# Kernel tuning notes

Measured on AMD Instinct MI355X. Metric: run time of the kernel, lower is better.

The kernel has to match this reference:

```python
import jax, jax.numpy as jnp
import numpy as np
from jax import lax

D_TEMPORAL, D_INNER, D_STATE, D_CONV, DT_RANK = 2, 4, 16, 4, 1
EPS = 1e-5


def setup_inputs() -> dict:
    key = jax.random.key(0)
    ks = jax.random.split(key, 14)
    B, L = 16, 32768
    f = lambda k, s, scale=1.0: jax.random.normal(k, s, jnp.float32) * scale
    dt_b = float(np.log(np.expm1(0.01)))  # softplus^-1(0.01), typical dt init
    A_log = jnp.log(jnp.tile(jnp.arange(1, D_STATE + 1, dtype=jnp.float32), (D_INNER, 1)))
    return {
        "hidden_states": f(ks[0], (B, D_TEMPORAL, L)),
        "norm_w": jnp.ones((D_TEMPORAL,), jnp.float32),
        "in_proj_w": f(ks[1], (2 * D_INNER, D_TEMPORAL), 0.5),
        "conv_w": f(ks[2], (D_INNER, D_CONV), 0.3),
        "conv_b": f(ks[3], (D_INNER,), 0.1),
        "x_proj_w": f(ks[4], (DT_RANK + 2 * D_STATE, D_INNER), 0.3),
        "dt_proj_w": f(ks[5], (D_INNER, DT_RANK), 1.0),
        "dt_proj_b": jnp.full((D_INNER,), dt_b, jnp.float32),
        "A_log": A_log,
        "D": jnp.ones((D_INNER,), jnp.float32),
        "conv_w_b": f(ks[6], (D_INNER, D_CONV), 0.3),
        "conv_b_b": f(ks[7], (D_INNER,), 0.1),
        "x_proj_w_b": f(ks[8], (DT_RANK + 2 * D_STATE, D_INNER), 0.3),
        "dt_proj_w_b": f(ks[9], (D_INNER, DT_RANK), 1.0),
        "dt_proj_b_b": jnp.full((D_INNER,), dt_b, jnp.float32),
        "A_b_log": A_log,
        "D_b": jnp.ones((D_INNER,), jnp.float32),
        "out_proj_w": f(ks[10], (D_TEMPORAL, D_INNER), 0.3),
        "norm_f_w": jnp.ones((D_TEMPORAL,), jnp.float32),
    }


def _silu(x):
    return x * jax.nn.sigmoid(x)


def _rmsnorm(x, w):
    return x * lax.rsqrt(jnp.mean(x * x, axis=-1, keepdims=True) + EPS) * w


def _branch(x, z, conv_w, conv_b, x_proj_w, dt_proj_w, dt_proj_b, A_log, D):
    # x, z: (B, d_inner, L). Causal depthwise conv + silu.
    Bb, d, L = x.shape
    xc = lax.conv_general_dilated(
        x, conv_w[:, None, :], (1,), [(D_CONV - 1, 0)],
        feature_group_count=d, dimension_numbers=("NCH", "OIH", "NCH"))
    u = _silu(xc + conv_b[None, :, None]).transpose(0, 2, 1)      # (B, L, d)
    x_dbl = u @ x_proj_w.T                                        # (B, L, rank+2n)
    dt, Bm, Cm = jnp.split(x_dbl, [DT_RANK, DT_RANK + D_STATE], axis=-1)
    dt = jax.nn.softplus(dt @ dt_proj_w.T + dt_proj_b)            # (B, L, d)
    A = -jnp.exp(A_log)                                           # (d, n)
    dA = jnp.exp(dt[..., None] * A)                               # (B, L, d, n)
    dBu = (dt * u)[..., None] * Bm[:, :, None, :]                 # (B, L, d, n)

    def step(h, inp):
        dA_t, dBu_t, C_t = inp
        h = dA_t * h + dBu_t                                      # (B, d, n)
        return h, jnp.einsum("bdn,bn->bd", h, C_t)

    h0 = jnp.zeros((Bb, d, D_STATE), dtype=u.dtype)
    _, ys = lax.scan(step, h0, (jnp.swapaxes(dA, 0, 1), jnp.swapaxes(dBu, 0, 1), jnp.swapaxes(Cm, 0, 1)))
    y = jnp.swapaxes(ys, 0, 1) + u * D                            # (B, L, d)
    return y * _silu(z.transpose(0, 2, 1))


def _forward(hidden_states, norm_w, in_proj_w, conv_w, conv_b, x_proj_w, dt_proj_w,
             dt_proj_b, A_log, D, conv_w_b, conv_b_b, x_proj_w_b, dt_proj_w_b,
             dt_proj_b_b, A_b_log, D_b, out_proj_w, norm_f_w):
    # hidden_states: (B, T=d_temporal, L); scan runs over L.
    hs = jnp.swapaxes(hidden_states, 1, 2)                        # (B, L, T)
    residual = hs.astype(jnp.float32)
    hs = _rmsnorm(residual, norm_w)
    xz = jnp.swapaxes(hs @ in_proj_w.T, 1, 2)                     # (B, 2*d_inner, L)
    x, z = jnp.split(xz, 2, axis=1)
    y_f = _branch(x, z, conv_w, conv_b, x_proj_w, dt_proj_w, dt_proj_b, A_log, D)
    y_b = _branch(x[..., ::-1], z[..., ::-1], conv_w_b, conv_b_b, x_proj_w_b,
                  dt_proj_w_b, dt_proj_b_b, A_b_log, D_b)
    y = y_f + y_b[:, ::-1, :]                                     # (B, L, d_inner)
    out = y @ out_proj_w.T                                        # (B, L, T)
    out = _rmsnorm(out + residual, norm_f_w)
    return jnp.swapaxes(out, 1, 2)                                # (B, T, L)


def reference(hidden_states, norm_w, in_proj_w, conv_w, conv_b, x_proj_w, dt_proj_w,
              dt_proj_b, A_log, D, conv_w_b, conv_b_b, x_proj_w_b, dt_proj_w_b,
              dt_proj_b_b, A_b_log, D_b, out_proj_w, norm_f_w):
    return _forward(hidden_states, norm_w, in_proj_w, conv_w, conv_b, x_proj_w,
                    dt_proj_w, dt_proj_b, A_log, D, conv_w_b, conv_b_b, x_proj_w_b,
                    dt_proj_w_b, dt_proj_b_b, A_b_log, D_b, out_proj_w, norm_f_w)
```

## Files before the change

### kernel.cpp

```cpp
#include <hip/hip_runtime.h>
#include <cstdint>

#define BB 16
#define LL 32768
#define NC 512
#define NSPAN 32
#define SPLEN 16

#define WD_SZ 256
#define XPW 0
#define CVW 132
#define CVB 148
#define DTW 152
#define DTB 156
#define AW  160
#define DW  224
#define G_INPROJ 512
#define G_NORMW 528
#define G_OUTP 530
#define G_NORMF 538
#define FLG 1000

#define PQ_OFF 4096
#define PQ_BYTES ((size_t)BB*2*NC*64*8)
#define SP_OFF (PQ_OFF + PQ_BYTES)
#define SP_BYTES ((size_t)BB*2*NSPAN*64*8)
#define WG_OFF (SP_OFF + SP_BYTES)
#define WG_BYTES ((size_t)BB*NC*2*64*64*2)
#define YB_OFF (WG_OFF + WG_BYTES)
#define YB_BYTES ((size_t)BB*NC*64*4*4)

#define LOG2E 1.4426950408889634f

__device__ __forceinline__ float bf2f(unsigned short u){ return __uint_as_float(((unsigned int)u)<<16); }
__device__ __forceinline__ float blo(unsigned int u){ return __uint_as_float(u<<16); }
__device__ __forceinline__ float bhi(unsigned int u){ return __uint_as_float(u & 0xffff0000u); }

__device__ __forceinline__ unsigned int cvtpk(float lo, float hi){
  unsigned int r;
  asm("v_cvt_pk_bf16_f32 %0, %1, %2" : "=v"(r) : "v"(lo), "v"(hi));
  return r;
}
__device__ __forceinline__ unsigned short cvt1(float x){
  return (unsigned short)cvtpk(x, x);
}

__device__ __forceinline__ float siluf(float x){ return x / (1.f + __expf(-x)); }
__device__ __forceinline__ float softplusf_(float x){ return fmaxf(x,0.f) + log1pf(__expf(-fabsf(x))); }

__device__ __forceinline__ float exp2fast(float x){
#if __has_builtin(__builtin_amdgcn_exp2f)
  return __builtin_amdgcn_exp2f(x);
#else
  float r; asm("v_exp_f32 %0, %1\ns_nop 0" : "=v"(r) : "v"(x)); return r;
#endif
}

__device__ __forceinline__ float rowsum16(float x){
  asm("s_nop 1\n\t"
      "v_add_f32_dpp %0, %0, %0 row_ror:1 row_mask:0xf bank_mask:0xf\n\t"
      "s_nop 1\n\t"
      "v_add_f32_dpp %0, %0, %0 row_ror:2 row_mask:0xf bank_mask:0xf\n\t"
      "s_nop 1\n\t"
      "v_add_f32_dpp %0, %0, %0 row_ror:4 row_mask:0xf bank_mask:0xf\n\t"
      "s_nop 1\n\t"
      "v_add_f32_dpp %0, %0, %0 row_ror:8 row_mask:0xf bank_mask:0xf"
      : "+v"(x));
  return x;
}

__device__ __forceinline__ float ldw(const void* p, int i, int isf){
  return isf ? ((const float*)p)[i] : bf2f(((const unsigned short*)p)[i]);
}
__device__ __forceinline__ float2 hid2(const void* hid, int isf, int b, int t){
  if (isf){
    const float* p = (const float*)hid;
    return make_float2(p[(size_t)b*2*LL + t], p[(size_t)b*2*LL + LL + t]);
  }
  const unsigned short* p = (const unsigned short*)hid;
  return make_float2(bf2f(p[(size_t)b*2*LL + t]), bf2f(p[(size_t)b*2*LL + LL + t]));
}
__device__ __forceinline__ float4 xrow(const void* __restrict__ hid, int isf,
                                       const float* __restrict__ W, int b, int t){
  float2 h = hid2(hid, isf, b, t);
  float ms = rsqrtf(0.5f*(h.x*h.x + h.y*h.y) + 1e-5f);
  float v0 = h.x*ms*W[G_NORMW], v1 = h.y*ms*W[G_NORMW+1];
  float4 x;
  x.x = W[G_INPROJ+0]*v0 + W[G_INPROJ+1]*v1;
  x.y = W[G_INPROJ+2]*v0 + W[G_INPROJ+3]*v1;
  x.z = W[G_INPROJ+4]*v0 + W[G_INPROJ+5]*v1;
  x.w = W[G_INPROJ+6]*v0 + W[G_INPROJ+7]*v1;
  return x;
}

__global__ void k_prep(const void* __restrict__ normw, const void* __restrict__ inpj,
    const void* __restrict__ cwf, const void* __restrict__ cbf,
    const void* __restrict__ xpf, const void* __restrict__ dwf,
    const void* __restrict__ dbf, const void* __restrict__ alf,
    const void* __restrict__ ddf,
    const void* __restrict__ cwb, const void* __restrict__ cbb,
    const void* __restrict__ xpb, const void* __restrict__ dwb,
    const void* __restrict__ dbb, const void* __restrict__ alb,
    const void* __restrict__ ddb,
    const void* __restrict__ outp, const void* __restrict__ nfw,
    float* __restrict__ W)
{
  const int isf = (((const unsigned int*)ddf)[0] == 0x3F800000u) ? 1 : 0;
  int t = threadIdx.x;
  for (int i=t;i<132;i+=256){ W[XPW+i]=ldw(xpf,i,isf); W[WD_SZ+XPW+i]=ldw(xpb,i,isf); }
  for (int i=t;i<16;i+=256){ W[CVW+i]=ldw(cwf,i,isf); W[WD_SZ+CVW+i]=ldw(cwb,i,isf); W[G_INPROJ+i]=ldw(inpj,i,isf); }
  for (int i=t;i<4;i+=256){
    W[CVB+i]=ldw(cbf,i,isf); W[WD_SZ+CVB+i]=ldw(cbb,i,isf);
    W[DTW+i]=ldw(dwf,i,isf); W[WD_SZ+DTW+i]=ldw(dwb,i,isf);
    W[DTB+i]=ldw(dbf,i,isf); W[WD_SZ+DTB+i]=ldw(dbb,i,isf);
    W[DW+i] =ldw(ddf,i,isf); W[WD_SZ+DW+i] =ldw(ddb,i,isf);
  }
  for (int i=t;i<64;i+=256){
    W[AW+i]       = -__expf(ldw(alf,i,isf)) * LOG2E;
    W[WD_SZ+AW+i] = -__expf(ldw(alb,i,isf)) * LOG2E;
  }
  for (int i=t;i<8;i+=256) W[G_OUTP+i]=ldw(outp,i,isf);
  for (int i=t;i<2;i+=256){ W[G_NORMW+i]=ldw(normw,i,isf); W[G_NORMF+i]=ldw(nfw,i,isf); }
  if (t==0) W[FLG] = (float)isf;
}

template<int DR>
__device__ __forceinline__ float2 scan_store(const float (* __restrict__ dtPd)[68],
    const unsigned short (* __restrict__ dtud)[68],
    const unsigned int (* __restrict__ bcd)[68],
    float (* __restrict__ ySd)[68],
    unsigned short* __restrict__ wrow,
    float Ax, int d, int n, int dn)
{
  unsigned short* wr   = wrow + dn;
  unsigned short* wrHi = wr + 32*64;
  float P = 1.f, h = 0.f;
  for (int j4=0; j4<16; j4++){
    const int t0 = DR ? 60-4*j4 : 4*j4;
    float4  d4 = *(const float4*)&dtPd[d][t0];
    ushort4 u4 = *(const ushort4*)&dtud[d][t0];
    uint4   c4 = *(const uint4*)&bcd[n][t0];
    float da[4]={d4.x,d4.y,d4.z,d4.w};
    unsigned short ua[4]={u4.x,u4.y,u4.z,u4.w};
    unsigned int ca[4]={c4.x,c4.y,c4.z,c4.w};
    float s[4];
    #pragma unroll
    for (int jr=0; jr<4; jr++){
      const int k  = DR ? 3-jr : jr;
      const int tt = t0 + k;
      float e = exp2fast(Ax*da[k]);
      P *= e;
      float Cf = bhi(ca[k]);
      h = fmaf(e, h, bf2f(ua[k])*blo(ca[k]));
      ((tt < 32) ? wr : wrHi)[(tt & 31)*64] = cvt1(P*Cf);
      s[k] = rowsum16(h*Cf);
    }
    if (n == 0) *(float4*)&ySd[d][t0] = make_float4(s[0],s[1],s[2],s[3]);
  }
  return make_float2(P, h);
}

__global__ __launch_bounds__(128, 4) void k_chunk2(const void* __restrict__ hid,
    const float* __restrict__ W, float2* __restrict__ PQ,
    unsigned short* __restrict__ Wg, float4* __restrict__ YB)
{
  __shared__ __align__(16) char smx[2176];
  __shared__ __align__(16) float dtP[2][4][68];
  __shared__ __align__(16) unsigned short dtuP[2][4][68];
  __shared__ __align__(16) unsigned int BCp[2][16][68];
  __shared__ __align__(16) float uD[2][256];
  float4* xb = (float4*)smx;
  float (*yS)[4][68] = (float (*)[4][68])smx;

  const int tid  = threadIdx.x;
  const int wid  = tid >> 6;
  const int lane = tid & 63;
  const int gid  = blockIdx.x;
  const int c    = gid & (NC-1);
  const int b    = gid >> 9;
  const int isf  = (int)W[FLG];

  if (wid == 0){
    int t = c*64 + lane;
    xb[lane+3] = xrow(hid, isf, W, b, t);
    if (lane < 3){
      int t2 = c*64 - 3 + lane;
      float4 v = make_float4(0.f,0.f,0.f,0.f);
      if (t2 >= 0) v = xrow(hid, isf, W, b, t2);
      xb[lane] = v;
    }
    if (lane >= 61){
      int t3 = c*64 + lane + 3;
      float4 v = make_float4(0.f,0.f,0.f,0.f);
      if (t3 < LL) v = xrow(hid, isf, W, b, t3);
      xb[lane+6] = v;
    }
  }
  __syncthreads();
  {
    const float* Wd = W + wid*WD_SZ;
    float4 a0,a1,a2,a3;
    if (wid == 0){ a0=xb[lane];   a1=xb[lane+1]; a2=xb[lane+2]; a3=xb[lane+3]; }
    else         { a0=xb[lane+6]; a1=xb[lane+5]; a2=xb[lane+4]; a3=xb[lane+3]; }
    float u[4];
    u[0] = siluf(Wd[CVB+0] + Wd[CVW+ 0]*a0.x + Wd[CVW+ 1]*a1.x + Wd[CVW+ 2]*a2.x + Wd[CVW+ 3]*a3.x);
    u[1] = siluf(Wd[CVB+1] + Wd[CVW+ 4]*a0.y + Wd[CVW+ 5]*a1.y + Wd[CVW+ 6]*a2.y + Wd[CVW+ 7]*a3.y);
    u[2] = siluf(Wd[CVB+2] + Wd[CVW+ 8]*a0.z + Wd[CVW+ 9]*a1.z + Wd[CVW+10]*a2.z + Wd[CVW+11]*a3.z);
    u[3] = siluf(Wd[CVB+3] + Wd[CVW+12]*a0.w + Wd[CVW+13]*a1.w + Wd[CVW+14]*a2.w + Wd[CVW+15]*a3.w);
    float dtr = Wd[XPW+0]*u[0] + Wd[XPW+1]*u[1] + Wd[XPW+2]*u[2] + Wd[XPW+3]*u[3];
    float4 ud4;
    #pragma unroll
    for (int d2=0; d2<4; d2++){
      float dt = softplusf_(fmaf(Wd[DTW+d2], dtr, Wd[DTB+d2]));
      dtP[wid][d2][lane]  = dt;
      dtuP[wid][d2][lane] = cvt1(dt*u[d2]);
      ((float*)&ud4)[d2] = u[d2]*Wd[DW+d2];
    }
    *(float4*)&uD[wid][lane*4] = ud4;
    #pragma unroll
    for (int n=0; n<16; n++){
      float Bn = Wd[XPW+(1+n)*4+0]*u[0] + Wd[XPW+(1+n)*4+1]*u[1]
               + Wd[XPW+(1+n)*4+2]*u[2] + Wd[XPW+(1+n)*4+3]*u[3];
      float Cn = Wd[XPW+(17+n)*4+0]*u[0] + Wd[XPW+(17+n)*4+1]*u[1]
               + Wd[XPW+(17+n)*4+2]*u[2] + Wd[XPW+(17+n)*4+3]*u[3];
      BCp[wid][n][lane] = cvtpk(Bn, Cn);
    }
  }
  __syncthreads();

  const int d = lane>>4, n = lane&15;
  const float Ax = W[wid*WD_SZ + AW + d*16 + n];
  unsigned short* wrow = Wg + ((size_t)gid*2 + wid)*64*64;
  float2 pq;
  size_t idx;
  if (wid == 0){
    pq  = scan_store<0>(dtP[0], dtuP[0], BCp[0], yS[0], wrow, Ax, d, n, lane);
    idx = ((size_t)(b*2+0)*NC + c);
  } else {
    pq  = scan_store<1>(dtP[1], dtuP[1], BCp[1], yS[1], wrow, Ax, d, n, lane);
    idx = ((size_t)(b*2+1)*NC + (NC-1-c));
  }
  PQ[idx*64 + lane] = pq;
  __syncthreads();

  if (wid == 0){
    float4 v;
    v.x = yS[0][0][lane] + yS[1][0][lane] + uD[0][lane*4+0] + uD[1][lane*4+0];
    v.y = yS[0][1][lane] + yS[1][1][lane] + uD[0][lane*4+1] + uD[1][lane*4+1];
    v.z = yS[0][2][lane] + yS[1][2][lane] + uD[0][lane*4+2] + uD[1][lane*4+2];
    v.w = yS[0][3][lane] + yS[1][3][lane] + uD[0][lane*4+3] + uD[1][lane*4+3];
    YB[(size_t)gid*64 + lane] = v;
  }
}

__global__ __launch_bounds__(64) void k_spans(const float2* __restrict__ PQ,
                                              float2* __restrict__ SP)
{
  const int blk  = blockIdx.x;
  const int lane = threadIdx.x;
  const int bd   = blk >> 5, span = blk & (NSPAN-1);
  const float2* p = PQ + ((size_t)bd*NC + span*SPLEN)*64 + lane;
  float2 v[SPLEN];
  #pragma unroll
  for (int k=0;k<SPLEN;k++) v[k] = p[k*64];
  float A = 1.f, Bc = 0.f;
  #pragma unroll
  for (int k=0;k<SPLEN;k++){ A *= v[k].x; Bc = fmaf(v[k].x, Bc, v[k].y); }
  SP[((size_t)bd*NSPAN + span)*64 + lane] = make_float2(A,Bc);
}

__device__ __forceinline__ float dot16(uint4 q0, uint4 q1, const float* h){
  float4 h0 = *(const float4*)(h+0),  h1 = *(const float4*)(h+4);
  float4 h2 = *(const float4*)(h+8),  h3 = *(const float4*)(h+12);
  float cacc = 0.f;
  cacc = fmaf(blo(q0.x), h0.x, cacc); cacc = fmaf(bhi(q0.x), h0.y, cacc);
  cacc = fmaf(blo(q0.y), h0.z, cacc); cacc = fmaf(bhi(q0.y), h0.w, cacc);
  cacc = fmaf(blo(q0.z), h1.x, cacc); cacc = fmaf(bhi(q0.z), h1.y, cacc);
  cacc = fmaf(blo(q0.w), h1.z, cacc); cacc = fmaf(bhi(q0.w), h1.w, cacc);
  cacc = fmaf(blo(q1.x), h2.x, cacc); cacc = fmaf(bhi(q1.x), h2.y, cacc);
  cacc = fmaf(blo(q1.y), h2.z, cacc); cacc = fmaf(bhi(q1.y), h2.w, cacc);
  cacc = fmaf(blo(q1.z), h3.x, cacc); cacc = fmaf(bhi(q1.z), h3.y, cacc);
  cacc = fmaf(blo(q1.w), h3.z, cacc); cacc = fmaf(bhi(q1.w), h3.w, cacc);
  return cacc;
}

__global__ __launch_bounds__(64) void k_final(const void* __restrict__ hid,
    const float* __restrict__ W, const float2* __restrict__ PQ,
    const float2* __restrict__ SP, const unsigned short* __restrict__ Wg,
    const float4* __restrict__ YB, void* __restrict__ out)
{
  __shared__ float h0s[2][64];
  const int lane = threadIdx.x;
  const int gid  = blockIdx.x;
  const int c    = gid & (NC-1);
  const int b    = gid >> 9;
  const int isf  = (int)W[FLG];

  #pragma unroll
  for (int dir=0; dir<2; dir++){
    const int p  = dir ? (NC-1-c) : c;
    const int bd = b*2 + dir;
    const int s  = p >> 4, wn = p & 15;
    const float2* SPb = SP + (size_t)bd*NSPAN*64 + lane;
    const float2* PQb = PQ + ((size_t)bd*NC + (p & ~15))*64 + lane;
    float h = 0.f;
    #pragma unroll
    for (int jg=0; jg<4; jg++){
      if (jg*8 < s){
        float2 v[8];
        #pragma unroll
        for (int j=0;j<8;j++){ int jj = jg*8+j; v[j] = SPb[(size_t)(jj<s?jj:0)*64]; }
        #pragma unroll
        for (int j=0;j<8;j++){ int jj = jg*8+j; if (jj<s) h = fmaf(v[j].x, h, v[j].y); }
      }
    }
    #pragma unroll
    for (int jg=0; jg<2; jg++){
      if (jg*8 < wn){
        float2 v[8];
        #pragma unroll
        for (int j=0;j<8;j++){ int jj = jg*8+j; v[j] = PQb[(size_t)(jj<wn?jj:0)*64]; }
        #pragma unroll
        for (int j=0;j<8;j++){ int jj = jg*8+j; if (jj<wn) h = fmaf(v[j].x, h, v[j].y); }
      }
    }
    h0s[dir][lane] = h;
  }
  __syncthreads();

  {
    const int t = lane;
    const uint4* wrF = (const uint4*)(Wg + (((size_t)gid*2 + 0)*64 + t)*64);
    const uint4* wrB = (const uint4*)(Wg + (((size_t)gid*2 + 1)*64 + t)*64);
    uint4 wf[8], wb[8];
    #pragma unroll
    for (int q=0;q<8;q++) wf[q] = wrF[q];
    #pragma unroll
    for (int q=0;q<8;q++) wb[q] = wrB[q];
    float4 yb = YB[(size_t)gid*64 + t];

    float corr[4];
    #pragma unroll
    for (int d2=0; d2<4; d2++){
      float cf = dot16(wf[d2*2], wf[d2*2+1], &h0s[0][d2*16]);
      float cb = dot16(wb[d2*2], wb[d2*2+1], &h0s[1][d2*16]);
      corr[d2] = cf + cb;
    }

    const int tg = c*64 + t;
    float2 r = hid2(hid, isf, b, tg);
    float ms0 = rsqrtf(0.5f*(r.x*r.x + r.y*r.y) + 1e-5f);
    float v0 = r.x*ms0*W[G_NORMW], v1 = r.y*ms0*W[G_NORMW+1];
    float z0 = siluf(W[G_INPROJ+ 8]*v0 + W[G_INPROJ+ 9]*v1);
    float z1 = siluf(W[G_INPROJ+10]*v0 + W[G_INPROJ+11]*v1);
    float z2 = siluf(W[G_INPROJ+12]*v0 + W[G_INPROJ+13]*v1);
    float z3 = siluf(W[G_INPROJ+14]*v0 + W[G_INPROJ+15]*v1);

    float y0 = (yb.x + corr[0]) * z0;
    float y1 = (yb.y + corr[1]) * z1;
    float y2 = (yb.z + corr[2]) * z2;
    float y3 = (yb.w + corr[3]) * z3;
    float o0 = W[G_OUTP+0]*y0 + W[G_OUTP+1]*y1 + W[G_OUTP+2]*y2 + W[G_OUTP+3]*y3;
    float o1 = W[G_OUTP+4]*y0 + W[G_OUTP+5]*y1 + W[G_OUTP+6]*y2 + W[G_OUTP+7]*y3;
    o0 += r.x;
    o1 += r.y;
    float ms = rsqrtf(0.5f*(o0*o0 + o1*o1) + 1e-5f);
    float e0 = o0*ms*W[G_NORMF], e1 = o1*ms*W[G_NORMF+1];
    size_t i0 = (size_t)b*2*LL + tg, i1 = i0 + LL;
    if (isf){
      ((float*)out)[i0] = e0;
      ((float*)out)[i1] = e1;
    } else {
      ((unsigned short*)out)[i0] = cvt1(e0);
      ((unsigned short*)out)[i1] = cvt1(e1);
    }
  }
}

extern "C" void kernel_launch(void* const* d_in, const int* in_sizes, int n_in,
                              void* d_out, int out_size, void* d_ws, size_t ws_size,
                              hipStream_t stream)
{
  (void)in_sizes; (void)n_in; (void)out_size; (void)ws_size;
  const void* hid   = d_in[0];
  const void* normw = d_in[1];
  const void* inpj  = d_in[2];
  const void* cwf   = d_in[3];
  const void* cbf   = d_in[4];
  const void* xpf   = d_in[5];
  const void* dwf   = d_in[6];
  const void* dbf   = d_in[7];
  const void* alf   = d_in[8];
  const void* ddf   = d_in[9];
  const void* cwb   = d_in[10];
  const void* cbb   = d_in[11];
  const void* xpb   = d_in[12];
  const void* dwb   = d_in[13];
  const void* dbb   = d_in[14];
  const void* alb   = d_in[15];
  const void* ddb   = d_in[16];
  const void* outp  = d_in[17];
  const void* nfw   = d_in[18];

  float* W            = (float*)d_ws;
  float2* PQ          = (float2*)((char*)d_ws + PQ_OFF);
  float2* SPt         = (float2*)((char*)d_ws + SP_OFF);
  unsigned short* Wg  = (unsigned short*)((char*)d_ws + WG_OFF);
  float4* YB          = (float4*)((char*)d_ws + YB_OFF);

  k_prep<<<1,256,0,stream>>>(normw, inpj, cwf, cbf, xpf, dwf, dbf, alf, ddf,
                             cwb, cbb, xpb, dwb, dbb, alb, ddb, outp, nfw, W);
  k_chunk2<<<BB*NC, 128, 0, stream>>>(hid, W, PQ, Wg, YB);
  k_spans<<<BB*2*NSPAN, 64, 0, stream>>>(PQ, SPt);
  k_final<<<BB*NC, 64, 0, stream>>>(hid, W, PQ, SPt, Wg, YB, d_out);
}
```

Baseline: 196.6 us.

## Split k_final across two waves per direction with LDS-staged coalesced Wg loads

k_final now runs 128 threads per block, with one wave per scan direction. Each wave computes its own direction's carry-in state and loads its 64x64 bf16 Wg matrix with coalesced uint4 reads. The matrix is staged through padded LDS and then read back row-wise for the per-position dot products. The previous version had each lane read a strided row directly from global memory. The two waves then share the correction results through LDS and each writes one output channel, at the cost of extra LDS use and an added barrier.

```diff
diff --git a/kernel.cpp b/kernel.cpp
--- a/kernel.cpp
+++ b/kernel.cpp
@@ -284,22 +284,31 @@
   return cacc;
 }
 
-__global__ __launch_bounds__(64) void k_final(const void* __restrict__ hid,
+#define WROW 72
+__global__ __launch_bounds__(128, 3) void k_final(const void* __restrict__ hid,
     const float* __restrict__ W, const float2* __restrict__ PQ,
     const float2* __restrict__ SP, const unsigned short* __restrict__ Wg,
     const float4* __restrict__ YB, void* __restrict__ out)
 {
   __shared__ float h0s[2][64];
-  const int lane = threadIdx.x;
+  __shared__ __align__(16) float yC[2][64][4];
+  __shared__ __align__(16) unsigned short Wt[2][64][WROW];
+  const int tid  = threadIdx.x;
+  const int wid  = tid >> 6;
+  const int lane = tid & 63;
   const int gid  = blockIdx.x;
   const int c    = gid & (NC-1);
   const int b    = gid >> 9;
   const int isf  = (int)W[FLG];
 
+  const uint4* gsrc = (const uint4*)(Wg + ((size_t)gid*2 + wid)*64*64);
+  uint4 st[8];
   #pragma unroll
-  for (int dir=0; dir<2; dir++){
-    const int p  = dir ? (NC-1-c) : c;
-    const int bd = b*2 + dir;
+  for (int i=0;i<8;i++) st[i] = gsrc[i*64 + lane];
+
+  {
+    const int p  = wid ? (NC-1-c) : c;
+    const int bd = b*2 + wid;
     const int s  = p >> 4, wn = p & 15;
     const float2* SPb = SP + (size_t)bd*NSPAN*64 + lane;
     const float2* PQb = PQ + ((size_t)bd*NC + (p & ~15))*64 + lane;
@@ -324,30 +333,35 @@
         for (int j=0;j<8;j++){ int jj = jg*8+j; if (jj<wn) h = fmaf(v[j].x, h, v[j].y); }
       }
     }
-    h0s[dir][lane] = h;
+    h0s[wid][lane] = h;
+  }
+
+  #pragma unroll
+  for (int i=0;i<8;i++){
+    int j = i*64 + lane;
+    *(uint4*)&Wt[wid][j>>3][(j&7)*8] = st[i];
   }
   __syncthreads();
 
   {
-    const int t = lane;
-    const uint4* wrF = (const uint4*)(Wg + (((size_t)gid*2 + 0)*64 + t)*64);
-    const uint4* wrB = (const uint4*)(Wg + (((size_t)gid*2 + 1)*64 + t)*64);
-    uint4 wf[8], wb[8];
-    #pragma unroll
-    for (int q=0;q<8;q++) wf[q] = wrF[q];
-    #pragma unroll
-    for (int q=0;q<8;q++) wb[q] = wrB[q];
+    uint4 wr_[8];
+    #pragma unroll
+    for (int q=0;q<8;q++) wr_[q] = *(const uint4*)&Wt[wid][lane][q*8];
+    float4 cr;
+    #pragma unroll
+    for (int d2=0; d2<4; d2++)
+      ((float*)&cr)[d2] = dot16(wr_[d2*2], wr_[d2*2+1], &h0s[wid][d2*16]);
+    *(float4*)&yC[wid][lane][0] = cr;
+  }
+  __syncthreads();
+
+  {
+    const int t  = lane;
+    const int tg = c*64 + t;
+    float4 cF = *(const float4*)&yC[0][t][0];
+    float4 cB = *(const float4*)&yC[1][t][0];
     float4 yb = YB[(size_t)gid*64 + t];
 
-    float corr[4];
-    #pragma unroll
-    for (int d2=0; d2<4; d2++){
-      float cf = dot16(wf[d2*2], wf[d2*2+1], &h0s[0][d2*16]);
-      float cb = dot16(wb[d2*2], wb[d2*2+1], &h0s[1][d2*16]);
-      corr[d2] = cf + cb;
-    }
-
-    const int tg = c*64 + t;
     float2 r = hid2(hid, isf, b, tg);
     float ms0 = rsqrtf(0.5f*(r.x*r.x + r.y*r.y) + 1e-5f);
     float v0 = r.x*ms0*W[G_NORMW], v1 = r.y*ms0*W[G_NORMW+1];
@@ -356,10 +370,10 @@
     float z2 = siluf(W[G_INPROJ+12]*v0 + W[G_INPROJ+13]*v1);
     float z3 = siluf(W[G_INPROJ+14]*v0 + W[G_INPROJ+15]*v1);
 
-    float y0 = (yb.x + corr[0]) * z0;
-    float y1 = (yb.y + corr[1]) * z1;
-    float y2 = (yb.z + corr[2]) * z2;
-    float y3 = (yb.w + corr[3]) * z3;
+    float y0 = (yb.x + cF.x + cB.x) * z0;
+    float y1 = (yb.y + cF.y + cB.y) * z1;
+    float y2 = (yb.z + cF.z + cB.z) * z2;
+    float y3 = (yb.w + cF.w + cB.w) * z3;
     float o0 = W[G_OUTP+0]*y0 + W[G_OUTP+1]*y1 + W[G_OUTP+2]*y2 + W[G_OUTP+3]*y3;
     float o1 = W[G_OUTP+4]*y0 + W[G_OUTP+5]*y1 + W[G_OUTP+6]*y2 + W[G_OUTP+7]*y3;
     o0 += r.x;
@@ -368,11 +382,11 @@
     float e0 = o0*ms*W[G_NORMF], e1 = o1*ms*W[G_NORMF+1];
     size_t i0 = (size_t)b*2*LL + tg, i1 = i0 + LL;
     if (isf){
-      ((float*)out)[i0] = e0;
-      ((float*)out)[i1] = e1;
+      if (wid == 0) ((float*)out)[i0] = e0;
+      else          ((float*)out)[i1] = e1;
     } else {
-      ((unsigned short*)out)[i0] = cvt1(e0);
-      ((unsigned short*)out)[i1] = cvt1(e1);
+      if (wid == 0) ((unsigned short*)out)[i0] = cvt1(e0);
+      else          ((unsigned short*)out)[i1] = cvt1(e1);
     }
   }
 }
@@ -412,5 +426,5 @@
                              cwb, cbb, xpb, dwb, dbb, alb, ddb, outp, nfw, W);
   k_chunk2<<<BB*NC, 128, 0, stream>>>(hid, W, PQ, Wg, YB);
   k_spans<<<BB*2*NSPAN, 64, 0, stream>>>(PQ, SPt);
-  k_final<<<BB*NC, 64, 0, stream>>>(hid, W, PQ, SPt, Wg, YB, d_out);
-}
+  k_final<<<BB*NC, 128, 0, stream>>>(hid, W, PQ, SPt, Wg, YB, d_out);
+}
```

After: 191.5 us. 2.6% less time.
